# Kernel optimization log

Measured on AMD Instinct MI355X. Metric: run time of the kernel, lower is better.

## Reference

```python
import jax, jax.numpy as jnp
import numpy as np


def setup_inputs() -> dict:
    key = jax.random.key(0)
    ks = jax.random.split(key, 5)
    B, S, C = 512, 512, 96
    emissions = jax.random.normal(ks[0], (B, S, C), dtype=jnp.float32)
    tags = jax.random.randint(ks[1], (B, S), 0, C, dtype=jnp.int64)
    masks = jnp.ones((B, S), dtype=bool)
    start_transitions = jax.random.uniform(ks[2], (C,), jnp.float32, -0.1, 0.1)
    end_transitions = jax.random.uniform(ks[3], (C,), jnp.float32, -0.1, 0.1)
    transitions = jax.random.uniform(ks[4], (C, C), jnp.float32, -0.1, 0.1)
    return {
        "emissions": emissions,
        "tags": tags,
        "masks": masks,
        "start_transitions": start_transitions,
        "end_transitions": end_transitions,
        "transitions": transitions,
    }


def _crf_llh(emissions, tags, masks, start_transitions, end_transitions, transitions):
    # to time-major: (S, B, C), (S, B)
    emissions = jnp.swapaxes(emissions, 0, 1)
    tags = jnp.swapaxes(tags, 0, 1)
    masks = jnp.swapaxes(masks, 0, 1)
    S, B, C = emissions.shape
    maskf = masks.astype(emissions.dtype)

    # ---- numerator: score of the gold tag path (fully vectorized over time) ----
    em_scores = jnp.take_along_axis(emissions, tags[:, :, None], axis=2)[:, :, 0]  # (S, B)
    trans_scores = transitions[tags[:-1], tags[1:]]  # (S-1, B)
    score = start_transitions[tags[0]] + em_scores[0]
    score = score + jnp.sum((trans_scores + em_scores[1:]) * maskf[1:], axis=0)
    seq_ends = masks.astype(jnp.int32).sum(axis=0) - 1  # (B,)
    last_tags = tags[seq_ends, jnp.arange(B)]
    numerator = score + end_transitions[last_tags]

    # ---- denominator: forward algorithm (sequential logsumexp recurrence) ----
    alpha0 = start_transitions[None, :] + emissions[0]  # (B, C)

    def step(alpha, inp):
        em_i, m_i = inp  # (B, C), (B,)
        # (B, C_prev, C_next)
        scores = alpha[:, :, None] + transitions[None, :, :] + em_i[:, None, :]
        next_alpha = jax.scipy.special.logsumexp(scores, axis=1)
        alpha = jnp.where(m_i[:, None], next_alpha, alpha)
        return alpha, None

    alpha, _ = jax.lax.scan(step, alpha0, (emissions[1:], masks[1:]))
    denominator = jax.scipy.special.logsumexp(alpha + end_transitions[None, :], axis=1)

    return jnp.mean(numerator - denominator)


def reference(emissions, tags, masks, start_transitions, end_transitions, transitions):
    return _crf_llh(emissions, tags, masks, start_transitions, end_transitions, transitions)
```

## Files before the change

kernel.cpp:

```cpp
#include <hip/hip_runtime.h>
#include <math.h>


#define BATCH 512
#define SEQ   512
#define NC    96
#define NTHR  256
#define CBYTES 208
#define GBYTES (NC * CBYTES)
#define LN2   0.69314718055994531f

typedef __fp16 half2v __attribute__((ext_vector_type(2)));
typedef __fp16 half8  __attribute__((ext_vector_type(8)));
typedef float  f32x4  __attribute__((ext_vector_type(4)));
typedef unsigned int uint2v __attribute__((ext_vector_type(2)));
typedef unsigned int uint4v __attribute__((ext_vector_type(4)));

#define BARRIER() asm volatile("s_waitcnt lgkmcnt(0)\n\ts_barrier" ::: "memory")

#define DPP_STEP_F(v, op, ctrl)                                              \
    v = op(v, __int_as_float(__builtin_amdgcn_update_dpp(                    \
            __float_as_int(v), __float_as_int(v), (ctrl), 0xf, 0xf, false)))

__device__ __forceinline__ float fadd_(float a, float b) { return a + b; }
__device__ __forceinline__ float wave_sum_all(float v) {
    DPP_STEP_F(v, fadd_, 0x111);
    DPP_STEP_F(v, fadd_, 0x112);
    DPP_STEP_F(v, fadd_, 0x114);
    DPP_STEP_F(v, fadd_, 0x118);
    DPP_STEP_F(v, fadd_, 0x142);
    DPP_STEP_F(v, fadd_, 0x143);
    return __int_as_float(__builtin_amdgcn_readlane(__float_as_int(v), 63));
}
__device__ __forceinline__ float wave_max_all(float v) {
    DPP_STEP_F(v, fmaxf, 0x111);
    DPP_STEP_F(v, fmaxf, 0x112);
    DPP_STEP_F(v, fmaxf, 0x114);
    DPP_STEP_F(v, fmaxf, 0x118);
    DPP_STEP_F(v, fmaxf, 0x142);
    DPP_STEP_F(v, fmaxf, 0x143);
    return __int_as_float(__builtin_amdgcn_readlane(__float_as_int(v), 63));
}

__device__ __forceinline__ unsigned pk2(float a, float b) {
    return __builtin_bit_cast(unsigned, __builtin_amdgcn_cvt_pkrtz(a, b));
}
__device__ __forceinline__ half2v bch(unsigned u) { return __builtin_bit_cast(half2v, u); }
__device__ __forceinline__ float fdot2_(unsigned a, unsigned b, float c) {
    return __builtin_amdgcn_fdot2(bch(a), bch(b), c, false);
}
__device__ __forceinline__ half8 h8(uint4v u) { return __builtin_bit_cast(half8, u); }
__device__ __forceinline__ half8 exp8(float4 u, float4 v) {
    uint4v r;
    r.x = pk2(__expf(u.x), __expf(u.y));
    r.y = pk2(__expf(u.z), __expf(u.w));
    r.z = pk2(__expf(v.x), __expf(v.y));
    r.w = pk2(__expf(v.z), __expf(v.w));
    return __builtin_bit_cast(half8, r);
}

__device__ __forceinline__ void coldot2(const char* colbase, const uint4v* sv,
                                        float& u0, float& u1) {
    float a0 = 0.f, a1 = 0.f, a2 = 0.f, a3 = 0.f;
    float b0 = 0.f, b1 = 0.f, b2 = 0.f, b3 = 0.f;
    #pragma unroll
    for (int q = 0; q < 12; ++q) {
        const uint4v x = *(const uint4v*)(colbase + 16 * q);
        const uint4v y = *(const uint4v*)(colbase + 48 * CBYTES + 16 * q);
        const uint4v s = sv[q];
        a0 = fdot2_(s.x, x.x, a0); a1 = fdot2_(s.y, x.y, a1);
        a2 = fdot2_(s.z, x.z, a2); a3 = fdot2_(s.w, x.w, a3);
        b0 = fdot2_(s.x, y.x, b0); b1 = fdot2_(s.y, y.y, b1);
        b2 = fdot2_(s.z, y.z, b2); b3 = fdot2_(s.w, y.w, b3);
    }
    u0 = (a0 + a1) + (a2 + a3);
    u1 = (b0 + b1) + (b2 + b3);
}

__global__ __launch_bounds__(256)
void exp_pre_kernel(const float* __restrict__ em, __fp16* __restrict__ ex) {
    const size_t i = ((size_t)blockIdx.x * 256 + threadIdx.x) * 8;
    const float4 a = *(const float4*)(em + i);
    const float4 b = *(const float4*)(em + i + 4);
    uint4v r;
    r.x = pk2(__expf(a.x), __expf(a.y));
    r.y = pk2(__expf(a.z), __expf(a.w));
    r.z = pk2(__expf(b.x), __expf(b.y));
    r.w = pk2(__expf(b.z), __expf(b.w));
    *(uint4v*)(ex + i) = r;
}

template<int UEX>
__global__ __launch_bounds__(NTHR, 2)
void crf_pair2_kernel(const float* __restrict__ em,
                      const int*   __restrict__ tags,
                      const int*   __restrict__ masks,
                      const float* __restrict__ startT,
                      const float* __restrict__ endT,
                      const float* __restrict__ trans,
                      const __fp16* __restrict__ exq,
                      float*       __restrict__ out)
{
    const int tid = threadIdx.x;
    const int l   = tid & 63;
    const int w   = tid >> 6;
    const int b   = blockIdx.x;

    __shared__ __align__(16) char  GBm[2][GBYTES];
    __shared__ __align__(16) char  EBm[GBYTES];
    __shared__ __align__(16) __fp16 ST[96];

    const float*  em_b    = em    + (size_t)b * SEQ * NC;
    const int*    masks_b = masks + (size_t)b * SEQ;
    const __fp16* exq_b   = UEX ? (exq + (size_t)b * SEQ * NC) : (const __fp16*)0;

    if (w == 0) {
        const bool act = (l < 48);

        float s0 = -1e30f, s1 = -1e30f;
        if (act) {
            s0 = startT[l]      + em_b[l];
            s1 = startT[l + 48] + em_b[l + 48];
        }
        const float M0 = wave_max_all(fmaxf(s0, s1));
        if (act) {
            ST[l]      = (__fp16)__expf(s0 - M0);
            ST[l + 48] = (__fp16)__expf(s1 - M0);
        }
        int sk = 0;

        auto ldE = [&](int row, float& x0, float& x1) {
            if (act) {
                if (UEX) {
                    x0 = (float)exq_b[(size_t)row * NC + l];
                    x1 = (float)exq_b[(size_t)row * NC + l + 48];
                } else {
                    x0 = __expf(em_b[(size_t)row * NC + l]);
                    x1 = __expf(em_b[(size_t)row * NC + l + 48]);
                }
            } else { x0 = 0.f; x1 = 0.f; }
        };

        auto sstep = [&](int row) {
            uint4v sv[12];
            const uint4v* stp = (const uint4v*)ST;
            #pragma unroll
            for (int q = 0; q < 12; ++q) sv[q] = stp[q];
            float v0 = 0.f, v1 = 0.f;
            if (act) coldot2((const char*)EBm + l * CBYTES, sv, v0, v1);
            if (act) {
                v0 *= __expf(em_b[(size_t)row * NC + l]);
                v1 *= __expf(em_b[(size_t)row * NC + l + 48]);
            }
            const float mx = wave_max_all(fmaxf(v0, v1));
            const unsigned ebx = (__float_as_uint(mx) >> 23) & 255u;
            sk += (int)ebx - 127;
            const float sc = __uint_as_float((254u - ebx) << 23);
            if (act) {
                ST[l]      = (__fp16)(v0 * sc);
                ST[l + 48] = (__fp16)(v1 * sc);
            }
        };

        auto body = [&](int t, float e0, float e1, int mk) {
            BARRIER();
            uint4v sv[12];
            const uint4v* stp = (const uint4v*)ST;
            #pragma unroll
            for (int q = 0; q < 12; ++q) sv[q] = stp[q];
            float u0 = 0.f, u1 = 0.f;
            __builtin_amdgcn_s_setprio(1);
            if (act) coldot2((const char*)GBm[t & 1] + l * CBYTES, sv, u0, u1);
            __builtin_amdgcn_s_setprio(0);
            if (mk == 3) {
                u0 *= e0; u1 *= e1;
                const float mx = wave_max_all(fmaxf(u0, u1));
                const unsigned ebx = (__float_as_uint(mx) >> 23) & 255u;
                sk += (int)ebx - 127;
                const float sc = __uint_as_float((254u - ebx) << 23);
                if (act) {
                    ST[l]      = (__fp16)(u0 * sc);
                    ST[l + 48] = (__fp16)(u1 * sc);
                }
            } else {
                if (mk & 1) sstep(2 * t + 1);
                if (mk & 2) sstep(2 * t + 2);
            }
        };

        float eA0, eA1, eB0, eB1;
        ldE(2, eA0, eA1);
        int mkA = (masks_b[1] ? 1 : 0) | (masks_b[2] ? 2 : 0);
        ldE(4, eB0, eB1);
        int mkB = (masks_b[3] ? 1 : 0) | (masks_b[4] ? 2 : 0);

        #pragma unroll 1
        for (int t = 0; t < 254; t += 2) {
            body(t, eA0, eA1, mkA);
            {
                const int rb = 2 * t + 6;
                ldE(rb, eA0, eA1);
                mkA = (masks_b[2 * t + 5] ? 1 : 0) | (masks_b[rb] ? 2 : 0);
            }
            body(t + 1, eB0, eB1, mkB);
            {
                const int ra = 2 * t + 7;
                const int rb = (2 * t + 8 > 511) ? 511 : (2 * t + 8);
                ldE(rb, eB0, eB1);
                mkB = (masks_b[ra] ? 1 : 0) | (masks_b[rb] ? 2 : 0);
            }
        }
        body(254, eA0, eA1, mkA);

        {
            uint4v sv[12];
            const uint4v* stp = (const uint4v*)ST;
            #pragma unroll
            for (int q = 0; q < 12; ++q) sv[q] = stp[q];
            float u0 = 0.f, u1 = 0.f;
            if (act) coldot2((const char*)EBm + l * CBYTES, sv, u0, u1);
            float w0 = 0.f, w1 = 0.f;
            if (act) {
                if (masks_b[511]) {
                    u0 *= __expf(em_b[(size_t)511 * NC + l]);
                    u1 *= __expf(em_b[(size_t)511 * NC + l + 48]);
                } else {
                    u0 = (float)ST[l];
                    u1 = (float)ST[l + 48];
                }
                w0 = u0 * __expf(endT[l]);
                w1 = u1 * __expf(endT[l + 48]);
            }
            const float dv = wave_sum_all(w0 + w1);
            if (l == 0)
                atomicAdd(out, -(M0 + (float)sk * LN2 + __logf(dv)) * (1.0f / (float)BATCH));
        }
    } else {
        const int lidx = l & 15;
        const int g    = l >> 4;
        const int nt0  = 2 * (w - 1);

        half8 Ea[6][3];
        #pragma unroll
        for (int r = 0; r < 6; ++r)
            #pragma unroll
            for (int c = 0; c < 3; ++c) {
                half8 v;
                #pragma unroll
                for (int e = 0; e < 8; ++e)
                    v[e] = (__fp16)__expf(trans[(16 * r + lidx) * NC + 32 * c + 8 * g + e]);
                Ea[r][c] = v;
            }
        half8 Eb[3][2];
        #pragma unroll
        for (int c = 0; c < 3; ++c)
            #pragma unroll
            for (int ntL = 0; ntL < 2; ++ntL) {
                half8 v;
                #pragma unroll
                for (int e = 0; e < 8; ++e)
                    v[e] = (__fp16)__expf(trans[(32 * c + 8 * g + e) * NC + 16 * (nt0 + ntL) + lidx]);
                Eb[c][ntL] = v;
            }
        #pragma unroll
        for (int ntL = 0; ntL < 2; ++ntL)
            #pragma unroll
            for (int c = 0; c < 3; ++c)
                *(uint4v*)(EBm + (16 * (nt0 + ntL) + lidx) * CBYTES + (4 * c + g) * 16) =
                    __builtin_bit_cast(uint4v, Eb[c][ntL]);

        auto build = [&](int bsel, half8 d0, half8 d1, half8 d2) {
            half8 bw[3][2];
            #pragma unroll
            for (int ntL = 0; ntL < 2; ++ntL) {
                bw[0][ntL] = Eb[0][ntL] * d0;
                bw[1][ntL] = Eb[1][ntL] * d1;
                bw[2][ntL] = Eb[2][ntL] * d2;
            }
            char* dst = GBm[bsel];
            #pragma unroll
            for (int ntL = 0; ntL < 2; ++ntL) {
                char* cp = dst + (16 * (nt0 + ntL) + lidx) * CBYTES
                               + 16 * (g >> 1) + 8 * (g & 1);
                #pragma unroll
                for (int r = 0; r < 6; ++r) {
                    const f32x4 z = {0.f, 0.f, 0.f, 0.f};
                    f32x4 acc = __builtin_amdgcn_mfma_f32_16x16x32_f16(Ea[r][0], bw[0][ntL], z, 0, 0, 0);
                    acc = __builtin_amdgcn_mfma_f32_16x16x32_f16(Ea[r][1], bw[1][ntL], acc, 0, 0, 0);
                    acc = __builtin_amdgcn_mfma_f32_16x16x32_f16(Ea[r][2], bw[2][ntL], acc, 0, 0, 0);
                    uint2v wv;
                    wv.x = pk2(acc[0], acc[1]);
                    wv.y = pk2(acc[2], acc[3]);
                    *(uint2v*)(cp + 32 * r) = wv;
                }
            }
        };

        if (UEX) {
            auto ld3 = [&](int row, uint4v& a, uint4v& bq, uint4v& c) {
                const char* p = (const char*)exq_b + (size_t)row * 192 + 16 * g;
                a  = *(const uint4v*)(p);
                bq = *(const uint4v*)(p + 64);
                c  = *(const uint4v*)(p + 128);
            };
            {
                uint4v a, bq, c;
                ld3(1, a, bq, c);
                build(0, h8(a), h8(bq), h8(c));
            }
            uint4v p0a, p0b, p0c, p1a, p1b, p1c;
            ld3(3, p0a, p0b, p0c);
            ld3(5, p1a, p1b, p1c);
            #pragma unroll 1
            for (int t = 0; t < 254; t += 2) {
                BARRIER();
                build(1, h8(p0a), h8(p0b), h8(p0c));
                { const int rr = 2 * t + 7; ld3(rr > 511 ? 511 : rr, p0a, p0b, p0c); }
                BARRIER();
                build(0, h8(p1a), h8(p1b), h8(p1c));
                { const int rr = 2 * t + 9; ld3(rr > 511 ? 511 : rr, p1a, p1b, p1c); }
            }
            BARRIER();
        } else {
            auto ld6 = [&](int row, float4& x0, float4& x1, float4& x2,
                           float4& x3, float4& x4, float4& x5) {
                const float* p = em_b + (size_t)row * NC + 8 * g;
                x0 = *(const float4*)(p);      x1 = *(const float4*)(p + 4);
                x2 = *(const float4*)(p + 32); x3 = *(const float4*)(p + 36);
                x4 = *(const float4*)(p + 64); x5 = *(const float4*)(p + 68);
            };
            {
                float4 x0, x1, x2, x3, x4, x5;
                ld6(1, x0, x1, x2, x3, x4, x5);
                build(0, exp8(x0, x1), exp8(x2, x3), exp8(x4, x5));
            }
            float4 a0, a1, a2, a3, a4, a5, b0, b1, b2, b3, b4, b5;
            ld6(3, a0, a1, a2, a3, a4, a5);
            ld6(5, b0, b1, b2, b3, b4, b5);
            #pragma unroll 1
            for (int t = 0; t < 254; t += 2) {
                BARRIER();
                build(1, exp8(a0, a1), exp8(a2, a3), exp8(a4, a5));
                { const int rr = 2 * t + 7; ld6(rr > 511 ? 511 : rr, a0, a1, a2, a3, a4, a5); }
                BARRIER();
                build(0, exp8(b0, b1), exp8(b2, b3), exp8(b4, b5));
                { const int rr = 2 * t + 9; ld6(rr > 511 ? 511 : rr, b0, b1, b2, b3, b4, b5); }
            }
            BARRIER();
        }

        if (w == 1) {
            const int* tb = tags + (size_t)b * SEQ;
            float nsum = 0.f, msum = 0.f;
            #pragma unroll
            for (int kk = 0; kk < 8; ++kk) {
                const int s  = l + 64 * kk;
                const int tg = tb[s];
                const int mk = masks_b[s];
                msum += mk ? 1.f : 0.f;
                if (s == 0) {
                    nsum += startT[tg] + em_b[tg];
                } else if (mk) {
                    nsum += trans[tb[s - 1] * NC + tg] + em_b[(size_t)s * NC + tg];
                }
            }
            nsum = wave_sum_all(nsum);
            msum = wave_sum_all(msum);
            if (l == 0) {
                const int cnt  = (int)msum;
                const int last = tb[cnt - 1];
                atomicAdd(out, (nsum + endT[last]) * (1.0f / (float)BATCH));
            }
        }
    }
}

extern "C" void kernel_launch(void* const* d_in, const int* in_sizes, int n_in,
                              void* d_out, int out_size, void* d_ws, size_t ws_size,
                              hipStream_t stream) {
    const float* em     = (const float*)d_in[0];
    const int*   tags   = (const int*)  d_in[1];
    const int*   masks  = (const int*)  d_in[2];
    const float* startT = (const float*)d_in[3];
    const float* endT   = (const float*)d_in[4];
    const float* trans  = (const float*)d_in[5];
    float* out = (float*)d_out;

    (void)hipMemsetAsync(out, 0, sizeof(float), stream);

    const size_t exbytes = (size_t)BATCH * SEQ * NC * sizeof(__fp16);
    if (d_ws != nullptr && ws_size >= exbytes) {
        const int nelem8 = BATCH * SEQ * NC / 8;
        exp_pre_kernel<<<nelem8 / 256, 256, 0, stream>>>(em, (__fp16*)d_ws);
        crf_pair2_kernel<1><<<BATCH, NTHR, 0, stream>>>(
            em, tags, masks, startT, endT, trans, (const __fp16*)d_ws, out);
    } else {
        crf_pair2_kernel<0><<<BATCH, NTHR, 0, stream>>>(
            em, tags, masks, startT, endT, trans, (const __fp16*)0, out);
    }
}
```

Measured before the change: 483.9 us.

## Fold four recurrence steps per serial iteration using products of transition matrices

The serial wave 0 recurrence now advances four time steps per iteration instead of two. Helper waves use MFMA to build a four-step product matrix from pair products PB1/PB2, with fixed scale factors to avoid fp16 overflow, into double-buffered HB. This halves the latency-bound serial dot-product chain and its barriers, at the cost of more MFMA work in the helper waves, more LDS use, and extra fp16 rounding over chained products. The masked fallback path now recomputes exp(trans) per step.

```diff
diff --git a/kernel.cpp b/kernel.cpp
--- a/kernel.cpp
+++ b/kernel.cpp
@@ -7,7 +7,7 @@
 #define NC    96
 #define NTHR  256
 #define CBYTES 208
-#define GBYTES (NC * CBYTES)
+#define PBYTES (NC * CBYTES)
 #define LN2   0.69314718055994531f
 
 typedef __fp16 half2v __attribute__((ext_vector_type(2)));
@@ -46,35 +46,21 @@
     return __builtin_bit_cast(unsigned, __builtin_amdgcn_cvt_pkrtz(a, b));
 }
 __device__ __forceinline__ half2v bch(unsigned u) { return __builtin_bit_cast(half2v, u); }
+__device__ __forceinline__ half8 h8(uint4v u) { return __builtin_bit_cast(half8, u); }
 __device__ __forceinline__ float fdot2_(unsigned a, unsigned b, float c) {
     return __builtin_amdgcn_fdot2(bch(a), bch(b), c, false);
 }
-__device__ __forceinline__ half8 h8(uint4v u) { return __builtin_bit_cast(half8, u); }
-__device__ __forceinline__ half8 exp8(float4 u, float4 v) {
-    uint4v r;
-    r.x = pk2(__expf(u.x), __expf(u.y));
-    r.y = pk2(__expf(u.z), __expf(u.w));
-    r.z = pk2(__expf(v.x), __expf(v.y));
-    r.w = pk2(__expf(v.z), __expf(v.w));
-    return __builtin_bit_cast(half8, r);
-}
-
-__device__ __forceinline__ void coldot2(const char* colbase, const uint4v* sv,
-                                        float& u0, float& u1) {
+__device__ __forceinline__ float dotcol(const char* colbase, const uint4v* sv) {
     float a0 = 0.f, a1 = 0.f, a2 = 0.f, a3 = 0.f;
-    float b0 = 0.f, b1 = 0.f, b2 = 0.f, b3 = 0.f;
     #pragma unroll
     for (int q = 0; q < 12; ++q) {
         const uint4v x = *(const uint4v*)(colbase + 16 * q);
-        const uint4v y = *(const uint4v*)(colbase + 48 * CBYTES + 16 * q);
-        const uint4v s = sv[q];
-        a0 = fdot2_(s.x, x.x, a0); a1 = fdot2_(s.y, x.y, a1);
-        a2 = fdot2_(s.z, x.z, a2); a3 = fdot2_(s.w, x.w, a3);
-        b0 = fdot2_(s.x, y.x, b0); b1 = fdot2_(s.y, y.y, b1);
-        b2 = fdot2_(s.z, y.z, b2); b3 = fdot2_(s.w, y.w, b3);
+        a0 = fdot2_(sv[q].x, x.x, a0);
+        a1 = fdot2_(sv[q].y, x.y, a1);
+        a2 = fdot2_(sv[q].z, x.z, a2);
+        a3 = fdot2_(sv[q].w, x.w, a3);
     }
-    u0 = (a0 + a1) + (a2 + a3);
-    u1 = (b0 + b1) + (b2 + b3);
+    return (a0 + a1) + (a2 + a3);
 }
 
 __global__ __launch_bounds__(256)
@@ -92,22 +78,23 @@
 
 template<int UEX>
 __global__ __launch_bounds__(NTHR, 2)
-void crf_pair2_kernel(const float* __restrict__ em,
-                      const int*   __restrict__ tags,
-                      const int*   __restrict__ masks,
-                      const float* __restrict__ startT,
-                      const float* __restrict__ endT,
-                      const float* __restrict__ trans,
-                      const __fp16* __restrict__ exq,
-                      float*       __restrict__ out)
+void crf_quad_kernel(const float* __restrict__ em,
+                     const int*   __restrict__ tags,
+                     const int*   __restrict__ masks,
+                     const float* __restrict__ startT,
+                     const float* __restrict__ endT,
+                     const float* __restrict__ trans,
+                     const __fp16* __restrict__ exq,
+                     float*       __restrict__ out)
 {
     const int tid = threadIdx.x;
     const int l   = tid & 63;
     const int w   = tid >> 6;
     const int b   = blockIdx.x;
 
-    __shared__ __align__(16) char  GBm[2][GBYTES];
-    __shared__ __align__(16) char  EBm[GBYTES];
+    __shared__ __align__(16) char  PB1[PBYTES];
+    __shared__ __align__(16) char  PB2[PBYTES];
+    __shared__ __align__(16) char  HB[2][PBYTES];
     __shared__ __align__(16) __fp16 ST[96];
 
     const float*  em_b    = em    + (size_t)b * SEQ * NC;
@@ -141,16 +128,16 @@
             } else { x0 = 0.f; x1 = 0.f; }
         };
 
-        auto sstep = [&](int row) {
-            uint4v sv[12];
-            const uint4v* stp = (const uint4v*)ST;
-            #pragma unroll
-            for (int q = 0; q < 12; ++q) sv[q] = stp[q];
+        auto sstep = [&](int s) {
             float v0 = 0.f, v1 = 0.f;
-            if (act) coldot2((const char*)EBm + l * CBYTES, sv, v0, v1);
             if (act) {
-                v0 *= __expf(em_b[(size_t)row * NC + l]);
-                v1 *= __expf(em_b[(size_t)row * NC + l + 48]);
+                for (int i = 0; i < NC; ++i) {
+                    const float wi = (float)ST[i];
+                    v0 += wi * __expf(trans[i * NC + l]);
+                    v1 += wi * __expf(trans[i * NC + l + 48]);
+                }
+                v0 *= __expf(em_b[(size_t)s * NC + l]);
+                v1 *= __expf(em_b[(size_t)s * NC + l + 48]);
             }
             const float mx = wave_max_all(fmaxf(v0, v1));
             const unsigned ebx = (__float_as_uint(mx) >> 23) & 255u;
@@ -162,7 +149,14 @@
             }
         };
 
-        auto body = [&](int t, float e0, float e1, int mk) {
+        float eC0, eC1;
+        ldE(4, eC0, eC1);
+        int m1 = masks_b[1], m2 = masks_b[2], m3 = masks_b[3], m4 = masks_b[4];
+
+        BARRIER();
+
+        #pragma unroll 1
+        for (int p = 0; p <= 127; ++p) {
             BARRIER();
             uint4v sv[12];
             const uint4v* stp = (const uint4v*)ST;
@@ -170,68 +164,50 @@
             for (int q = 0; q < 12; ++q) sv[q] = stp[q];
             float u0 = 0.f, u1 = 0.f;
             __builtin_amdgcn_s_setprio(1);
-            if (act) coldot2((const char*)GBm[t & 1] + l * CBYTES, sv, u0, u1);
+            if (act) {
+                const char* hb = HB[p & 1];
+                u0 = dotcol(hb + l * CBYTES, sv);
+                u1 = dotcol(hb + (l + 48) * CBYTES, sv);
+            }
             __builtin_amdgcn_s_setprio(0);
-            if (mk == 3) {
-                u0 *= e0; u1 *= e1;
+            BARRIER();
+            const bool last = (p == 127);
+            const bool fast = last ? (m1 && m2 && m3) : (m1 && m2 && m3 && m4);
+            if (fast) {
+                u0 *= eC0; u1 *= eC1;
                 const float mx = wave_max_all(fmaxf(u0, u1));
                 const unsigned ebx = (__float_as_uint(mx) >> 23) & 255u;
-                sk += (int)ebx - 127;
+                sk += (int)ebx - 127 + (last ? 8 : 15);
                 const float sc = __uint_as_float((254u - ebx) << 23);
                 if (act) {
                     ST[l]      = (__fp16)(u0 * sc);
                     ST[l + 48] = (__fp16)(u1 * sc);
                 }
             } else {
-                if (mk & 1) sstep(2 * t + 1);
-                if (mk & 2) sstep(2 * t + 2);
-            }
-        };
-
-        float eA0, eA1, eB0, eB1;
-        ldE(2, eA0, eA1);
-        int mkA = (masks_b[1] ? 1 : 0) | (masks_b[2] ? 2 : 0);
-        ldE(4, eB0, eB1);
-        int mkB = (masks_b[3] ? 1 : 0) | (masks_b[4] ? 2 : 0);
-
-        #pragma unroll 1
-        for (int t = 0; t < 254; t += 2) {
-            body(t, eA0, eA1, mkA);
-            {
-                const int rb = 2 * t + 6;
-                ldE(rb, eA0, eA1);
-                mkA = (masks_b[2 * t + 5] ? 1 : 0) | (masks_b[rb] ? 2 : 0);
-            }
-            body(t + 1, eB0, eB1, mkB);
-            {
-                const int ra = 2 * t + 7;
-                const int rb = (2 * t + 8 > 511) ? 511 : (2 * t + 8);
-                ldE(rb, eB0, eB1);
-                mkB = (masks_b[ra] ? 1 : 0) | (masks_b[rb] ? 2 : 0);
-            }
-        }
-        body(254, eA0, eA1, mkA);
+                const int ns = last ? 3 : 4;
+                for (int j = 0; j < ns; ++j) {
+                    const int s = 4 * p + 1 + j;
+                    const int mkj = (j == 0) ? m1 : (j == 1) ? m2 : (j == 2) ? m3 : m4;
+                    if (mkj) sstep(s);
+                }
+            }
+            if (p < 127) {
+                const int pn = p + 1;
+                ldE((pn == 127) ? 511 : (4 * pn + 4), eC0, eC1);
+                m1 = masks_b[4 * pn + 1];
+                m2 = masks_b[4 * pn + 2];
+                m3 = masks_b[4 * pn + 3];
+                m4 = (pn == 127) ? 1 : masks_b[4 * pn + 4];
+            }
+        }
 
         {
-            uint4v sv[12];
-            const uint4v* stp = (const uint4v*)ST;
-            #pragma unroll
-            for (int q = 0; q < 12; ++q) sv[q] = stp[q];
-            float u0 = 0.f, u1 = 0.f;
-            if (act) coldot2((const char*)EBm + l * CBYTES, sv, u0, u1);
-            float w0 = 0.f, w1 = 0.f;
+            float d0 = 0.f, d1 = 0.f;
             if (act) {
-                if (masks_b[511]) {
-                    u0 *= __expf(em_b[(size_t)511 * NC + l]);
-                    u1 *= __expf(em_b[(size_t)511 * NC + l + 48]);
-                } else {
-                    u0 = (float)ST[l];
-                    u1 = (float)ST[l + 48];
-                }
-                w0 = u0 * __expf(endT[l]);
-                w1 = u1 * __expf(endT[l + 48]);
-            }
-            const float dv = wave_sum_all(w0 + w1);
+                d0 = (float)ST[l]      * __expf(endT[l]);
+                d1 = (float)ST[l + 48] * __expf(endT[l + 48]);
+            }
+            const float dv = wave_sum_all(d0 + d1);
             if (l == 0)
                 atomicAdd(out, -(M0 + (float)sk * LN2 + __logf(dv)) * (1.0f / (float)BATCH));
         }
@@ -240,113 +216,143 @@
         const int g    = l >> 4;
         const int nt0  = 2 * (w - 1);
 
-        half8 Ea[6][3];
+        half8 RowF[6][3], ColF[6][3];
         #pragma unroll
         for (int r = 0; r < 6; ++r)
             #pragma unroll
             for (int c = 0; c < 3; ++c) {
-                half8 v;
-                #pragma unroll
-                for (int e = 0; e < 8; ++e)
-                    v[e] = (__fp16)__expf(trans[(16 * r + lidx) * NC + 32 * c + 8 * g + e]);
-                Ea[r][c] = v;
-            }
-        half8 Eb[3][2];
-        #pragma unroll
-        for (int c = 0; c < 3; ++c)
+                half8 va, vb;
+                #pragma unroll
+                for (int e = 0; e < 8; ++e) {
+                    va[e] = (__fp16)__expf(trans[(16 * r + lidx) * NC + 32 * c + 8 * g + e]);
+                    vb[e] = (__fp16)__expf(trans[(32 * c + 8 * g + e) * NC + 16 * r + lidx]);
+                }
+                RowF[r][c] = va;
+                ColF[r][c] = vb;
+            }
+
+        const half8 SC7 = { (__fp16)0.0078125f, (__fp16)0.0078125f, (__fp16)0.0078125f, (__fp16)0.0078125f,
+                            (__fp16)0.0078125f, (__fp16)0.0078125f, (__fp16)0.0078125f, (__fp16)0.0078125f };
+        const half8 SC1 = { (__fp16)0.5f, (__fp16)0.5f, (__fp16)0.5f, (__fp16)0.5f,
+                            (__fp16)0.5f, (__fp16)0.5f, (__fp16)0.5f, (__fp16)0.5f };
+
+        auto ldd = [&](int row, uint4v d[3]) {
+            if (UEX) {
+                const char* p = (const char*)exq_b + (size_t)row * 192 + 16 * g;
+                d[0] = *(const uint4v*)(p);
+                d[1] = *(const uint4v*)(p + 64);
+                d[2] = *(const uint4v*)(p + 128);
+            } else {
+                const float* p = em_b + (size_t)row * NC + 8 * g;
+                #pragma unroll
+                for (int c = 0; c < 3; ++c) {
+                    const float4 a = *(const float4*)(p + 32 * c);
+                    const float4 bq = *(const float4*)(p + 32 * c + 4);
+                    uint4v r_;
+                    r_.x = pk2(__expf(a.x), __expf(a.y));
+                    r_.y = pk2(__expf(a.z), __expf(a.w));
+                    r_.z = pk2(__expf(bq.x), __expf(bq.y));
+                    r_.w = pk2(__expf(bq.z), __expf(bq.w));
+                    d[c] = r_;
+                }
+            }
+        };
+
+        auto buildP = [&](const uint4v dA[3], const uint4v dB[3], bool tail) {
+            half8 dAs[3], dBs[3];
+            #pragma unroll
+            for (int c = 0; c < 3; ++c) { dAs[c] = h8(dA[c]) * SC7; dBs[c] = h8(dB[c]) * SC7; }
+            const f32x4 z = {0.f, 0.f, 0.f, 0.f};
             #pragma unroll
             for (int ntL = 0; ntL < 2; ++ntL) {
-                half8 v;
-                #pragma unroll
-                for (int e = 0; e < 8; ++e)
-                    v[e] = (__fp16)__expf(trans[(32 * c + 8 * g + e) * NC + 16 * (nt0 + ntL) + lidx]);
-                Eb[c][ntL] = v;
-            }
-        #pragma unroll
-        for (int ntL = 0; ntL < 2; ++ntL)
-            #pragma unroll
-            for (int c = 0; c < 3; ++c)
-                *(uint4v*)(EBm + (16 * (nt0 + ntL) + lidx) * CBYTES + (4 * c + g) * 16) =
-                    __builtin_bit_cast(uint4v, Eb[c][ntL]);
-
-        auto build = [&](int bsel, half8 d0, half8 d1, half8 d2) {
-            half8 bw[3][2];
+                const int nt = nt0 + ntL;
+                half8 b0 = dAs[0] * RowF[nt][0];
+                half8 b1 = dAs[1] * RowF[nt][1];
+                half8 b2 = dAs[2] * RowF[nt][2];
+                char* cp = PB1 + (16 * nt + lidx) * CBYTES + 8 * g;
+                #pragma unroll
+                for (int r = 0; r < 6; ++r) {
+                    f32x4 acc = __builtin_amdgcn_mfma_f32_16x16x32_f16(ColF[r][0], b0, z, 0, 0, 0);
+                    acc = __builtin_amdgcn_mfma_f32_16x16x32_f16(ColF[r][1], b1, acc, 0, 0, 0);
+                    acc = __builtin_amdgcn_mfma_f32_16x16x32_f16(ColF[r][2], b2, acc, 0, 0, 0);
+                    uint2v wv; wv.x = pk2(acc[0], acc[1]); wv.y = pk2(acc[2], acc[3]);
+                    *(uint2v*)(cp + 32 * r) = wv;
+                }
+            }
+            if (!tail) {
+                #pragma unroll
+                for (int ntL = 0; ntL < 2; ++ntL) {
+                    const int nt = nt0 + ntL;
+                    half8 b0 = dBs[0] * ColF[nt][0];
+                    half8 b1 = dBs[1] * ColF[nt][1];
+                    half8 b2 = dBs[2] * ColF[nt][2];
+                    char* cp = PB2 + (16 * nt + lidx) * CBYTES + 8 * g;
+                    #pragma unroll
+                    for (int r = 0; r < 6; ++r) {
+                        f32x4 acc = __builtin_amdgcn_mfma_f32_16x16x32_f16(RowF[r][0], b0, z, 0, 0, 0);
+                        acc = __builtin_amdgcn_mfma_f32_16x16x32_f16(RowF[r][1], b1, acc, 0, 0, 0);
+                        acc = __builtin_amdgcn_mfma_f32_16x16x32_f16(RowF[r][2], b2, acc, 0, 0, 0);
+                        uint2v wv; wv.x = pk2(acc[0], acc[1]); wv.y = pk2(acc[2], acc[3]);
+                        *(uint2v*)(cp + 32 * r) = wv;
+                    }
+                }
+            }
+        };
+
+        auto buildH = [&](const uint4v dC[3], int hsel, bool tail) {
+            half8 dCs[3];
+            #pragma unroll
+            for (int c = 0; c < 3; ++c) dCs[c] = h8(dC[c]) * SC1;
+            half8 Bf[2][3];
             #pragma unroll
             for (int ntL = 0; ntL < 2; ++ntL) {
-                bw[0][ntL] = Eb[0][ntL] * d0;
-                bw[1][ntL] = Eb[1][ntL] * d1;
-                bw[2][ntL] = Eb[2][ntL] * d2;
-            }
-            char* dst = GBm[bsel];
-            #pragma unroll
-            for (int ntL = 0; ntL < 2; ++ntL) {
-                char* cp = dst + (16 * (nt0 + ntL) + lidx) * CBYTES
-                               + 16 * (g >> 1) + 8 * (g & 1);
-                #pragma unroll
-                for (int r = 0; r < 6; ++r) {
-                    const f32x4 z = {0.f, 0.f, 0.f, 0.f};
-                    f32x4 acc = __builtin_amdgcn_mfma_f32_16x16x32_f16(Ea[r][0], bw[0][ntL], z, 0, 0, 0);
-                    acc = __builtin_amdgcn_mfma_f32_16x16x32_f16(Ea[r][1], bw[1][ntL], acc, 0, 0, 0);
-                    acc = __builtin_amdgcn_mfma_f32_16x16x32_f16(Ea[r][2], bw[2][ntL], acc, 0, 0, 0);
-                    uint2v wv;
-                    wv.x = pk2(acc[0], acc[1]);
-                    wv.y = pk2(acc[2], acc[3]);
-                    *(uint2v*)(cp + 32 * r) = wv;
+                const int nt = nt0 + ntL;
+                #pragma unroll
+                for (int c = 0; c < 3; ++c) {
+                    if (tail) Bf[ntL][c] = ColF[nt][c];
+                    else      Bf[ntL][c] = h8(*(const uint4v*)(PB2 + (16 * nt + lidx) * CBYTES + 64 * c + 16 * g));
+                }
+            }
+            const f32x4 z = {0.f, 0.f, 0.f, 0.f};
+            char* hb = HB[hsel];
+            #pragma unroll
+            for (int r = 0; r < 6; ++r) {
+                const char* ap = PB1 + (16 * r + lidx) * CBYTES + 16 * g;
+                const half8 A0 = h8(*(const uint4v*)(ap))       * dCs[0];
+                const half8 A1 = h8(*(const uint4v*)(ap + 64))  * dCs[1];
+                const half8 A2 = h8(*(const uint4v*)(ap + 128)) * dCs[2];
+                #pragma unroll
+                for (int ntL = 0; ntL < 2; ++ntL) {
+                    f32x4 acc = __builtin_amdgcn_mfma_f32_16x16x32_f16(A0, Bf[ntL][0], z, 0, 0, 0);
+                    acc = __builtin_amdgcn_mfma_f32_16x16x32_f16(A1, Bf[ntL][1], acc, 0, 0, 0);
+                    acc = __builtin_amdgcn_mfma_f32_16x16x32_f16(A2, Bf[ntL][2], acc, 0, 0, 0);
+                    uint2v wv; wv.x = pk2(acc[0], acc[1]); wv.y = pk2(acc[2], acc[3]);
+                    *(uint2v*)(hb + (16 * (nt0 + ntL) + lidx) * CBYTES + 32 * r + 8 * g) = wv;
                 }
             }
         };
 
-        if (UEX) {
-            auto ld3 = [&](int row, uint4v& a, uint4v& bq, uint4v& c) {
-                const char* p = (const char*)exq_b + (size_t)row * 192 + 16 * g;
-                a  = *(const uint4v*)(p);
-                bq = *(const uint4v*)(p + 64);
-                c  = *(const uint4v*)(p + 128);
-            };
-            {
-                uint4v a, bq, c;
-                ld3(1, a, bq, c);
-                build(0, h8(a), h8(bq), h8(c));
-            }
-            uint4v p0a, p0b, p0c, p1a, p1b, p1c;
-            ld3(3, p0a, p0b, p0c);
-            ld3(5, p1a, p1b, p1c);
-            #pragma unroll 1
-            for (int t = 0; t < 254; t += 2) {
-                BARRIER();
-                build(1, h8(p0a), h8(p0b), h8(p0c));
-                { const int rr = 2 * t + 7; ld3(rr > 511 ? 511 : rr, p0a, p0b, p0c); }
-                BARRIER();
-                build(0, h8(p1a), h8(p1b), h8(p1c));
-                { const int rr = 2 * t + 9; ld3(rr > 511 ? 511 : rr, p1a, p1b, p1c); }
-            }
+        uint4v dA[3], dB[3], dC[3], nA[3], nB[3], nC[3];
+        ldd(1, dA); ldd(3, dB); ldd(2, dC);
+        buildP(dA, dB, false);
+        ldd(5, nA); ldd(7, nB); ldd(6, nC);
+        BARRIER();
+        buildH(dC, 0, false);
+
+        #pragma unroll 1
+        for (int p = 0; p <= 127; ++p) {
             BARRIER();
-        } else {
-            auto ld6 = [&](int row, float4& x0, float4& x1, float4& x2,
-                           float4& x3, float4& x4, float4& x5) {
-                const float* p = em_b + (size_t)row * NC + 8 * g;
-                x0 = *(const float4*)(p);      x1 = *(const float4*)(p + 4);
-                x2 = *(const float4*)(p + 32); x3 = *(const float4*)(p + 36);
-                x4 = *(const float4*)(p + 64); x5 = *(const float4*)(p + 68);
-            };
-            {
-                float4 x0, x1, x2, x3, x4, x5;
-                ld6(1, x0, x1, x2, x3, x4, x5);
-                build(0, exp8(x0, x1), exp8(x2, x3), exp8(x4, x5));
-            }
-            float4 a0, a1, a2, a3, a4, a5, b0, b1, b2, b3, b4, b5;
-            ld6(3, a0, a1, a2, a3, a4, a5);
-            ld6(5, b0, b1, b2, b3, b4, b5);
-            #pragma unroll 1
-            for (int t = 0; t < 254; t += 2) {
-                BARRIER();
-                build(1, exp8(a0, a1), exp8(a2, a3), exp8(a4, a5));
-                { const int rr = 2 * t + 7; ld6(rr > 511 ? 511 : rr, a0, a1, a2, a3, a4, a5); }
-                BARRIER();
-                build(0, exp8(b0, b1), exp8(b2, b3), exp8(b4, b5));
-                { const int rr = 2 * t + 9; ld6(rr > 511 ? 511 : rr, b0, b1, b2, b3, b4, b5); }
+            const int q = p + 1;
+            #pragma unroll
+            for (int c = 0; c < 3; ++c) { dA[c] = nA[c]; dB[c] = nB[c]; dC[c] = nC[c]; }
+            if (q <= 127) buildP(dA, dB, q == 127);
+            if (q <= 126) {
+                const int qq = q + 1;
+                const int rb = (4 * qq + 3 > 511) ? 511 : (4 * qq + 3);
+                ldd(4 * qq + 1, nA); ldd(rb, nB); ldd(4 * qq + 2, nC);
             }
             BARRIER();
+            if (q <= 127) buildH(dC, q & 1, q == 127);
         }
 
         if (w == 1) {
@@ -392,10 +398,10 @@
     if (d_ws != nullptr && ws_size >= exbytes) {
         const int nelem8 = BATCH * SEQ * NC / 8;
         exp_pre_kernel<<<nelem8 / 256, 256, 0, stream>>>(em, (__fp16*)d_ws);
-        crf_pair2_kernel<1><<<BATCH, NTHR, 0, stream>>>(
+        crf_quad_kernel<1><<<BATCH, NTHR, 0, stream>>>(
             em, tags, masks, startT, endT, trans, (const __fp16*)d_ws, out);
     } else {
-        crf_pair2_kernel<0><<<BATCH, NTHR, 0, stream>>>(
+        crf_quad_kernel<0><<<BATCH, NTHR, 0, stream>>>(
             em, tags, masks, startT, endT, trans, (const __fp16*)0, out);
     }
 }
```

Result: slower. 665.4 us (+37.5%).
